# Kernel tuning notes

Measured on AMD Instinct MI355X. Metric: run time of the kernel, lower is better.

The kernel has to match this reference:

```python
import jax, jax.numpy as jnp
import numpy as np

N_QUBITS = 10
N_LAYERS = 4
BATCH = 512
FREQS = (1.0, 2.0, 4.0, 8.0, 16.0)
PI = float(np.pi)

# Combined CZ @ CNOT on (control, target), basis order |ct>
_CZCNOT = jnp.array([[1, 0, 0, 0],
                     [0, 1, 0, 0],
                     [0, 0, 0, -1],
                     [0, 0, 1, 0]], dtype=jnp.complex64)


def _apply_1q(state, U, q):
    # state: [B, 2,...,2]; U: [B,2,2] batched single-qubit gate on wire q
    s = jnp.moveaxis(state, q + 1, -1)
    s = jnp.einsum('b...i,bji->b...j', s, U)
    return jnp.moveaxis(s, -1, q + 1)


def _rz(state, phi, q):
    # diagonal gate: just multiply phases on the target axis
    s = jnp.moveaxis(state, q + 1, -1)
    h = phi * 0.5
    ph = jnp.stack([jnp.exp(-1j * h), jnp.exp(1j * h)], axis=-1).astype(jnp.complex64)  # [B,2]
    ph = ph.reshape(ph.shape[0], *([1] * (s.ndim - 2)), 2)
    return jnp.moveaxis(s * ph, -1, q + 1)


def _rx(state, th, q):
    c = jnp.cos(th * 0.5).astype(jnp.complex64)
    s_ = (-1j * jnp.sin(th * 0.5)).astype(jnp.complex64)
    U = jnp.stack([jnp.stack([c, s_], -1), jnp.stack([s_, c], -1)], -2)  # [B,2,2]
    return _apply_1q(state, U, q)


def _ry(state, th, q):
    c = jnp.cos(th * 0.5).astype(jnp.complex64)
    s_ = jnp.sin(th * 0.5).astype(jnp.complex64)
    U = jnp.stack([jnp.stack([c, -s_], -1), jnp.stack([s_, c], -1)], -2)
    return _apply_1q(state, U, q)


def _apply_2q(state, U4, c, t):
    # constant 4x4 gate on wires (c, t)
    s = jnp.moveaxis(state, (c + 1, t + 1), (-2, -1))
    shp = s.shape
    s = s.reshape(shp[:-2] + (4,))
    s = jnp.einsum('...i,ji->...j', s, U4)
    s = s.reshape(shp)
    return jnp.moveaxis(s, (-2, -1), (c + 1, t + 1))


def _forward(inputs, theta):
    B = inputs.shape[0]
    x = jnp.tanh(inputs)  # [B, n_feat]
    n_feat = x.shape[1]
    # |0...0> batched statevector [B, 2,...,2]
    state = jnp.zeros((B,) + (2,) * N_QUBITS, jnp.complex64)
    state = state.at[(slice(None),) + (0,) * N_QUBITS].set(1.0)
    # Fourier feature map: RZ(f*x), RX(0.5*f*x) per wire per frequency
    for q in range(N_QUBITS):
        xi = x[:, q % n_feat]
        for f in FREQS:
            state = _rz(state, f * xi, q)
            state = _rx(state, f * xi * 0.5, q)
    ang = jnp.tanh(theta) * PI  # [L, n, 3]
    for layer in range(N_LAYERS):
        for q in range(N_QUBITS):
            a = ang[layer, q]
            # qml.Rot(a0,a1,a2) = RZ(a0) -> RY(a1) -> RZ(a2), then RX(0.5*a0)
            state = _rz(state, jnp.broadcast_to(a[0], (B,)), q)
            state = _ry(state, jnp.broadcast_to(a[1], (B,)), q)
            state = _rz(state, jnp.broadcast_to(a[2], (B,)), q)
            state = _rx(state, jnp.broadcast_to(a[0] * 0.5, (B,)), q)
        for q in range(0, N_QUBITS - 1, 2):
            state = _apply_2q(state, _CZCNOT, q, q + 1)
        for q in range(1, N_QUBITS - 1, 2):
            state = _apply_2q(state, _CZCNOT, q, q + 1)
    # <Z_q> from probabilities
    p = jnp.abs(state) ** 2  # [B, 2,...,2] real
    exps = []
    for q in range(N_QUBITS):
        axes = tuple(a for a in range(1, N_QUBITS + 1) if a != q + 1)
        m = p.sum(axis=axes)  # [B,2]
        exps.append(m[:, 0] - m[:, 1])
    return jnp.stack(exps, axis=1).astype(jnp.float32)  # [B, n_qubits]


def setup_inputs() -> dict:
    key = jax.random.key(0)
    k1, k2 = jax.random.split(key)
    inputs = jax.random.normal(k1, (BATCH, N_QUBITS), dtype=jnp.float32)
    theta = jax.random.normal(k2, (N_LAYERS, N_QUBITS, 3), dtype=jnp.float32) * 0.1
    return {"inputs": inputs, "theta": theta}


def reference(inputs, theta):
    return _forward(inputs, theta)
```

## Files before the change

kernel.cpp:

```cpp
#include <hip/hip_runtime.h>
#include <math.h>

#define PI_F 3.14159265358979323846f

__device__ __forceinline__ float2 cmul(float2 a, float2 b) {
    return make_float2(a.x * b.x - a.y * b.y, a.x * b.y + a.y * b.x);
}
__device__ __forceinline__ float2 cfma(float2 u, float2 v, float2 acc) {
    acc.x = fmaf(u.x, v.x, fmaf(-u.y, v.y, acc.x));
    acc.y = fmaf(u.x, v.y, fmaf(u.y, v.x, acc.y));
    return acc;
}

__device__ __forceinline__ void gate_b0(float2 a[4], const float2* U) {
    float2 u00 = U[0], u01 = U[1], u10 = U[2], u11 = U[3];
    float2 n0 = cfma(u00, a[0], cmul(u01, a[1]));
    float2 n1 = cfma(u10, a[0], cmul(u11, a[1]));
    float2 n2 = cfma(u00, a[2], cmul(u01, a[3]));
    float2 n3 = cfma(u10, a[2], cmul(u11, a[3]));
    a[0] = n0; a[1] = n1; a[2] = n2; a[3] = n3;
}
__device__ __forceinline__ void gate_b1(float2 a[4], const float2* U) {
    float2 u00 = U[0], u01 = U[1], u10 = U[2], u11 = U[3];
    float2 n0 = cfma(u00, a[0], cmul(u01, a[2]));
    float2 n2 = cfma(u10, a[0], cmul(u11, a[2]));
    float2 n1 = cfma(u00, a[1], cmul(u01, a[3]));
    float2 n3 = cfma(u10, a[1], cmul(u11, a[3]));
    a[0] = n0; a[1] = n1; a[2] = n2; a[3] = n3;
}
__device__ __forceinline__ void gate_lane(float2 a[4], const float2* U, int p, int l) {
    int mask = 1 << p;
    bool h = (l >> p) & 1;
    float2 al = h ? U[3] : U[0];
    float2 be = h ? U[2] : U[1];
    #pragma unroll
    for (int r = 0; r < 4; r++) {
        float2 pa;
        pa.x = __shfl_xor(a[r].x, mask, 64);
        pa.y = __shfl_xor(a[r].y, mask, 64);
        a[r] = cfma(al, a[r], cmul(be, pa));
    }
}

__global__ __launch_bounds__(256) void qsim_fused(const float* __restrict__ inputs,
                                                  const float* __restrict__ theta,
                                                  float* __restrict__ out) {
    const int b = blockIdx.x;
    const int T = threadIdx.x;
    const int l = T & 63;
    const int w = T >> 6;

    __shared__ float2 sm[40][4];
    __shared__ float2 ve[10][2];
    __shared__ float2 vq[10][2];
    __shared__ float2 m4s[4][16];
    __shared__ __align__(16) float2 xch[2][1024];
    __shared__ float red[4][10];

    if (T < 40) {
        float a0 = tanhf(theta[T * 3 + 0]) * PI_F;
        float a1 = tanhf(theta[T * 3 + 1]) * PI_F;
        float a2 = tanhf(theta[T * 3 + 2]) * PI_F;
        float sz0, cz0; sincosf(a0 * 0.5f, &sz0, &cz0);
        float2 m00 = make_float2(cz0, -sz0);
        float2 m11 = make_float2(cz0,  sz0);
        float sy, cy; sincosf(a1 * 0.5f, &sy, &cy);
        float2 t00 = make_float2(cy * m00.x, cy * m00.y);
        float2 t01 = make_float2(-sy * m11.x, -sy * m11.y);
        float2 t10 = make_float2(sy * m00.x, sy * m00.y);
        float2 t11 = make_float2(cy * m11.x, cy * m11.y);
        float sz2, cz2; sincosf(a2 * 0.5f, &sz2, &cz2);
        float2 e0 = make_float2(cz2, -sz2), e1 = make_float2(cz2, sz2);
        t00 = cmul(e0, t00); t01 = cmul(e0, t01);
        t10 = cmul(e1, t10); t11 = cmul(e1, t11);
        float sx, cx; sincosf(a0 * 0.25f, &sx, &cx);
        sm[T][0] = make_float2(cx * t00.x + sx * t10.y, cx * t00.y - sx * t10.x);
        sm[T][1] = make_float2(cx * t01.x + sx * t11.y, cx * t01.y - sx * t11.x);
        sm[T][2] = make_float2(cx * t10.x + sx * t00.y, cx * t10.y - sx * t00.x);
        sm[T][3] = make_float2(cx * t11.x + sx * t01.y, cx * t11.y - sx * t01.x);
    } else if (T >= 64 && T < 74) {
        int q = T - 64;
        float x = tanhf(inputs[b * 10 + q]);
        float2 v0 = make_float2(1.f, 0.f), v1 = make_float2(0.f, 0.f);
        #pragma unroll
        for (int k = 0; k < 5; k++) {
            float phi = (float)(1 << k) * x;
            float sh, ch; sincosf(phi * 0.5f, &sh, &ch);
            float2 n0 = cmul(make_float2(ch, -sh), v0);
            float2 n1 = cmul(make_float2(ch,  sh), v1);
            float sx, cxx; sincosf(phi * 0.25f, &sx, &cxx);
            v0 = make_float2(cxx * n0.x + sx * n1.y, cxx * n0.y - sx * n1.x);
            v1 = make_float2(cxx * n1.x + sx * n0.y, cxx * n1.y - sx * n0.x);
        }
        ve[q][0] = v0; ve[q][1] = v1;
    }
    __syncthreads();
    if (T < 48) {
        int li = T >> 4, lyr = li + 1;
        int e = T & 15, row = e >> 2, col = e & 3;
        int sr = (row == 2) ? 3 : (row == 3) ? 2 : row;
        float sgn = (row == 2) ? -1.f : 1.f;
        float2 u0 = sm[lyr * 10 + 0][(sr >> 1) * 2 + (col >> 1)];
        float2 u1 = sm[lyr * 10 + 1][(sr & 1) * 2 + (col & 1)];
        float2 p = cmul(u0, u1);
        m4s[lyr][e] = make_float2(sgn * p.x, sgn * p.y);
    } else if (T >= 64 && T < 74) {
        int q = T - 64;
        float2 v0 = ve[q][0], v1 = ve[q][1];
        vq[q][0] = cfma(sm[q][0], v0, cmul(sm[q][1], v1));
        vq[q][1] = cfma(sm[q][2], v0, cmul(sm[q][3], v1));
    }
    __syncthreads();

    const int i0 = (w << 8) | (l << 2);
    float2 a[4];
    {
        int ii = i0;
        int f1 = (ii & 0x154) >> 1; int m = ii ^ f1;
        int f2 = (m & 0x2AA) >> 1;  int sh = m ^ f2;
        float2 P = vq[7][(sh >> 2) & 1];
        P = cmul(P, vq[6][(sh >> 3) & 1]);
        P = cmul(P, vq[5][(sh >> 4) & 1]);
        P = cmul(P, vq[4][(sh >> 5) & 1]);
        P = cmul(P, vq[3][(sh >> 6) & 1]);
        P = cmul(P, vq[2][(sh >> 7) & 1]);
        P = cmul(P, vq[1][(sh >> 8) & 1]);
        P = cmul(P, vq[0][(sh >> 9) & 1]);
        #pragma unroll
        for (int r = 0; r < 4; r++) {
            int i = i0 | r;
            int g1 = (i & 0x154) >> 1; int mm = i ^ g1;
            int g2 = (mm & 0x2AA) >> 1; int s = mm ^ g2;
            int neg = (__popc(g1 & ~i) + __popc(g2 & ~mm)) & 1;
            float2 t = cmul(vq[8][(s >> 1) & 1], vq[9][s & 1]);
            t = cmul(P, t);
            a[r] = neg ? make_float2(-t.x, -t.y) : t;
        }
    }

    int srcLane;
    float sg0, sg1, sg2, sg3;
    {
        #define CZP(r, SG) { int i = i0 | r; int g1 = (i & 0x154) >> 1; int mm = i ^ g1; \
                             int g2 = (mm & 0xAA) >> 1; int s = mm ^ g2; \
                             int neg = (__popc(g1 & ~i) + __popc(g2 & ~mm)) & 1; \
                             SG = neg ? -1.f : 1.f; if (r == 0) srcLane = (s >> 2) & 63; }
        CZP(0, sg0) CZP(1, sg1) CZP(2, sg2) CZP(3, sg3)
        #undef CZP
    }
    const bool L0 = l & 1;

    #pragma unroll
    for (int L = 1; L < 4; L++) {
        const float2 (*G)[4] = (const float2(*)[4])&sm[L * 10 + 2];
        gate_lane(a, G[0], 5, l);
        gate_lane(a, G[1], 4, l);
        gate_lane(a, G[2], 3, l);
        gate_lane(a, G[3], 2, l);
        gate_lane(a, G[4], 1, l);
        gate_lane(a, G[5], 0, l);
        gate_b1(a, G[6]);
        gate_b0(a, G[7]);
        {
            int buf = L & 1;
            float4* wp = (float4*)&xch[buf][T << 2];
            wp[0] = make_float4(a[0].x, a[0].y, a[1].x, a[1].y);
            wp[1] = make_float4(a[2].x, a[2].y, a[3].x, a[3].y);
            __syncthreads();
            const float2* M4row = &m4s[L][w * 4];
            float2 mw = M4row[w];
            float2 n[4];
            #pragma unroll
            for (int r = 0; r < 4; r++) n[r] = cmul(mw, a[r]);
            #pragma unroll
            for (int j = 0; j < 3; j++) {
                int wo = (w + 1 + j) & 3;
                float2 c = M4row[wo];
                const float4* rp = (const float4*)&xch[buf][(wo << 8) | (l << 2)];
                float4 v0 = rp[0], v1 = rp[1];
                n[0] = cfma(c, make_float2(v0.x, v0.y), n[0]);
                n[1] = cfma(c, make_float2(v0.z, v0.w), n[1]);
                n[2] = cfma(c, make_float2(v1.x, v1.y), n[2]);
                n[3] = cfma(c, make_float2(v1.z, v1.w), n[3]);
            }
            a[0] = n[0]; a[1] = n[1]; a[2] = n[2]; a[3] = n[3];
        }
        {
            float p0x = __shfl(a[0].x, srcLane, 64), p0y = __shfl(a[0].y, srcLane, 64);
            float p1x = __shfl(a[1].x, srcLane, 64), p1y = __shfl(a[1].y, srcLane, 64);
            float p2x = __shfl(a[2].x, srcLane, 64), p2y = __shfl(a[2].y, srcLane, 64);
            float p3x = __shfl(a[3].x, srcLane, 64), p3y = __shfl(a[3].y, srcLane, 64);
            a[0] = make_float2(sg0 * (L0 ? p3x : p0x), sg0 * (L0 ? p3y : p0y));
            a[1] = make_float2(sg1 * (L0 ? p2x : p1x), sg1 * (L0 ? p2y : p1y));
            a[2] = make_float2(sg2 * (L0 ? p0x : p3x), sg2 * (L0 ? p0y : p3y));
            a[3] = make_float2(sg3 * (L0 ? p1x : p2x), sg3 * (L0 ? p1y : p2y));
        }
    }

    float p0 = a[0].x * a[0].x + a[0].y * a[0].y;
    float p1 = a[1].x * a[1].x + a[1].y * a[1].y;
    float p2 = a[2].x * a[2].x + a[2].y * a[2].y;
    float p3 = a[3].x * a[3].x + a[3].y * a[3].y;
    float S = p0 + p1 + p2 + p3;
    float e[10];
    e[9] = p0 - p1 + p2 - p3;
    e[8] = p0 + p1 - p2 - p3;
    #pragma unroll
    for (int q = 2; q <= 7; q++) e[q] = ((l >> (7 - q)) & 1) ? -S : S;
    e[1] = (w & 1) ? -S : S;
    e[0] = (w & 2) ? -S : S;
    #pragma unroll
    for (int q = 0; q < 10; q++) {
        float v = e[q];
        #pragma unroll
        for (int off = 32; off > 0; off >>= 1) v += __shfl_down(v, off, 64);
        e[q] = v;
    }
    if ((T & 63) == 0) {
        #pragma unroll
        for (int q = 0; q < 10; q++) red[w][q] = e[q];
    }
    __syncthreads();
    if (T < 10) {
        out[b * 10 + T] = red[0][T] + red[1][T] + red[2][T] + red[3][T];
    }
}

extern "C" void kernel_launch(void* const* d_in, const int* in_sizes, int n_in,
                              void* d_out, int out_size, void* d_ws, size_t ws_size,
                              hipStream_t stream) {
    const float* inputs = (const float*)d_in[0];
    const float* theta  = (const float*)d_in[1];
    float* out = (float*)d_out;
    qsim_fused<<<512, 256, 0, stream>>>(inputs, theta, out);
}
```

Before: 16.19 us.

## Use DPP and permlane cross-lane ops, butterfly reduction, drop final CZ signs

Replaces ds_bpermute-based shuffles for lane bits 0, 1 and 5 with DPP quad permutes and permlane32_swap. The final expectation reduction becomes a single xor-butterfly that builds all per-bit differences at once, replacing ten separate 6-step shuffle reductions. Other changes: the feature-map sincos calls are replaced by double-angle recurrences, the phase product is computed as a tree, and the sign multiply is skipped in the last layer since signs do not affect probabilities. The aim is to cut LDS-crossbar shuffle traffic and reduction instructions, at the cost of small precision drift from the angle recurrence.

```diff
diff --git a/kernel.cpp b/kernel.cpp
--- a/kernel.cpp
+++ b/kernel.cpp
@@ -2,6 +2,8 @@
 #include <math.h>
 
 #define PI_F 3.14159265358979323846f
+
+typedef unsigned u32v2 __attribute__((ext_vector_type(2)));
 
 __device__ __forceinline__ float2 cmul(float2 a, float2 b) {
     return make_float2(a.x * b.x - a.y * b.y, a.x * b.y + a.y * b.x);
@@ -12,6 +14,62 @@
     return acc;
 }
 
+__device__ __forceinline__ float dpp_x1(float x) {
+    return __int_as_float(__builtin_amdgcn_update_dpp(0, __float_as_int(x), 0xB1, 0xF, 0xF, true));
+}
+__device__ __forceinline__ float dpp_x2(float x) {
+    return __int_as_float(__builtin_amdgcn_update_dpp(0, __float_as_int(x), 0x4E, 0xF, 0xF, true));
+}
+#if __has_builtin(__builtin_amdgcn_permlane32_swap)
+__device__ __forceinline__ float pl32(float x, int l) {
+    unsigned u = __float_as_uint(x);
+    u32v2 r = __builtin_amdgcn_permlane32_swap(u, u, false, false);
+    return __uint_as_float((l & 32) ? r.x : r.y);
+}
+#else
+__device__ __forceinline__ float pl32(float x, int l) { return __shfl_xor(x, 32, 64); }
+#endif
+
+__device__ __forceinline__ void gate_apply(float2 a[4], const float2 pa[4], float2 al, float2 be) {
+    #pragma unroll
+    for (int r = 0; r < 4; r++) a[r] = cfma(al, a[r], cmul(be, pa[r]));
+}
+__device__ __forceinline__ void gate_dpp1(float2 a[4], const float2* U, int l) {
+    bool h = l & 1;
+    float2 al = h ? U[3] : U[0], be = h ? U[2] : U[1];
+    float2 pa[4];
+    #pragma unroll
+    for (int r = 0; r < 4; r++) { pa[r].x = dpp_x1(a[r].x); pa[r].y = dpp_x1(a[r].y); }
+    gate_apply(a, pa, al, be);
+}
+__device__ __forceinline__ void gate_dpp2(float2 a[4], const float2* U, int l) {
+    bool h = l & 2;
+    float2 al = h ? U[3] : U[0], be = h ? U[2] : U[1];
+    float2 pa[4];
+    #pragma unroll
+    for (int r = 0; r < 4; r++) { pa[r].x = dpp_x2(a[r].x); pa[r].y = dpp_x2(a[r].y); }
+    gate_apply(a, pa, al, be);
+}
+__device__ __forceinline__ void gate_pl32(float2 a[4], const float2* U, int l) {
+    bool h = l & 32;
+    float2 al = h ? U[3] : U[0], be = h ? U[2] : U[1];
+    float2 pa[4];
+    #pragma unroll
+    for (int r = 0; r < 4; r++) { pa[r].x = pl32(a[r].x, l); pa[r].y = pl32(a[r].y, l); }
+    gate_apply(a, pa, al, be);
+}
+__device__ __forceinline__ void gate_shfl(float2 a[4], const float2* U, int p, int l) {
+    int mask = 1 << p;
+    bool h = (l >> p) & 1;
+    float2 al = h ? U[3] : U[0], be = h ? U[2] : U[1];
+    float2 pa[4];
+    #pragma unroll
+    for (int r = 0; r < 4; r++) {
+        pa[r].x = __shfl_xor(a[r].x, mask, 64);
+        pa[r].y = __shfl_xor(a[r].y, mask, 64);
+    }
+    gate_apply(a, pa, al, be);
+}
 __device__ __forceinline__ void gate_b0(float2 a[4], const float2* U) {
     float2 u00 = U[0], u01 = U[1], u10 = U[2], u11 = U[3];
     float2 n0 = cfma(u00, a[0], cmul(u01, a[1]));
@@ -27,19 +85,6 @@
     float2 n1 = cfma(u00, a[1], cmul(u01, a[3]));
     float2 n3 = cfma(u10, a[1], cmul(u11, a[3]));
     a[0] = n0; a[1] = n1; a[2] = n2; a[3] = n3;
-}
-__device__ __forceinline__ void gate_lane(float2 a[4], const float2* U, int p, int l) {
-    int mask = 1 << p;
-    bool h = (l >> p) & 1;
-    float2 al = h ? U[3] : U[0];
-    float2 be = h ? U[2] : U[1];
-    #pragma unroll
-    for (int r = 0; r < 4; r++) {
-        float2 pa;
-        pa.x = __shfl_xor(a[r].x, mask, 64);
-        pa.y = __shfl_xor(a[r].y, mask, 64);
-        a[r] = cfma(al, a[r], cmul(be, pa));
-    }
 }
 
 __global__ __launch_bounds__(256) void qsim_fused(const float* __restrict__ inputs,
@@ -81,16 +126,22 @@
     } else if (T >= 64 && T < 74) {
         int q = T - 64;
         float x = tanhf(inputs[b * 10 + q]);
+        float sA[6], cA[6];
+        sincosf(0.25f * x, &sA[0], &cA[0]);
+        #pragma unroll
+        for (int j = 1; j < 6; j++) {
+            sA[j] = 2.f * sA[j - 1] * cA[j - 1];
+            cA[j] = 1.f - 2.f * sA[j - 1] * sA[j - 1];
+        }
         float2 v0 = make_float2(1.f, 0.f), v1 = make_float2(0.f, 0.f);
         #pragma unroll
         for (int k = 0; k < 5; k++) {
-            float phi = (float)(1 << k) * x;
-            float sh, ch; sincosf(phi * 0.5f, &sh, &ch);
+            float sh = sA[k + 1], ch = cA[k + 1];
             float2 n0 = cmul(make_float2(ch, -sh), v0);
             float2 n1 = cmul(make_float2(ch,  sh), v1);
-            float sx, cxx; sincosf(phi * 0.25f, &sx, &cxx);
-            v0 = make_float2(cxx * n0.x + sx * n1.y, cxx * n0.y - sx * n1.x);
-            v1 = make_float2(cxx * n1.x + sx * n0.y, cxx * n1.y - sx * n0.x);
+            float sx = sA[k], cx = cA[k];
+            v0 = make_float2(cx * n0.x + sx * n1.y, cx * n0.y - sx * n1.x);
+            v1 = make_float2(cx * n1.x + sx * n0.y, cx * n1.y - sx * n0.x);
         }
         ve[q][0] = v0; ve[q][1] = v1;
     }
@@ -115,17 +166,13 @@
     const int i0 = (w << 8) | (l << 2);
     float2 a[4];
     {
-        int ii = i0;
-        int f1 = (ii & 0x154) >> 1; int m = ii ^ f1;
+        int f1 = (i0 & 0x154) >> 1; int m = i0 ^ f1;
         int f2 = (m & 0x2AA) >> 1;  int sh = m ^ f2;
-        float2 P = vq[7][(sh >> 2) & 1];
-        P = cmul(P, vq[6][(sh >> 3) & 1]);
-        P = cmul(P, vq[5][(sh >> 4) & 1]);
-        P = cmul(P, vq[4][(sh >> 5) & 1]);
-        P = cmul(P, vq[3][(sh >> 6) & 1]);
-        P = cmul(P, vq[2][(sh >> 7) & 1]);
-        P = cmul(P, vq[1][(sh >> 8) & 1]);
-        P = cmul(P, vq[0][(sh >> 9) & 1]);
+        float2 t76 = cmul(vq[7][(sh >> 2) & 1], vq[6][(sh >> 3) & 1]);
+        float2 t54 = cmul(vq[5][(sh >> 4) & 1], vq[4][(sh >> 5) & 1]);
+        float2 t32 = cmul(vq[3][(sh >> 6) & 1], vq[2][(sh >> 7) & 1]);
+        float2 t10 = cmul(vq[1][(sh >> 8) & 1], vq[0][(sh >> 9) & 1]);
+        float2 P = cmul(cmul(t76, t54), cmul(t32, t10));
         #pragma unroll
         for (int r = 0; r < 4; r++) {
             int i = i0 | r;
@@ -148,17 +195,17 @@
         CZP(0, sg0) CZP(1, sg1) CZP(2, sg2) CZP(3, sg3)
         #undef CZP
     }
-    const bool L0 = l & 1;
+    const bool Lb = l & 1;
 
     #pragma unroll
     for (int L = 1; L < 4; L++) {
         const float2 (*G)[4] = (const float2(*)[4])&sm[L * 10 + 2];
-        gate_lane(a, G[0], 5, l);
-        gate_lane(a, G[1], 4, l);
-        gate_lane(a, G[2], 3, l);
-        gate_lane(a, G[3], 2, l);
-        gate_lane(a, G[4], 1, l);
-        gate_lane(a, G[5], 0, l);
+        gate_pl32(a, G[0], l);
+        gate_shfl(a, G[1], 4, l);
+        gate_shfl(a, G[2], 3, l);
+        gate_shfl(a, G[3], 2, l);
+        gate_dpp2(a, G[4], l);
+        gate_dpp1(a, G[5], l);
         gate_b1(a, G[6]);
         gate_b0(a, G[7]);
         {
@@ -190,10 +237,17 @@
             float p1x = __shfl(a[1].x, srcLane, 64), p1y = __shfl(a[1].y, srcLane, 64);
             float p2x = __shfl(a[2].x, srcLane, 64), p2y = __shfl(a[2].y, srcLane, 64);
             float p3x = __shfl(a[3].x, srcLane, 64), p3y = __shfl(a[3].y, srcLane, 64);
-            a[0] = make_float2(sg0 * (L0 ? p3x : p0x), sg0 * (L0 ? p3y : p0y));
-            a[1] = make_float2(sg1 * (L0 ? p2x : p1x), sg1 * (L0 ? p2y : p1y));
-            a[2] = make_float2(sg2 * (L0 ? p0x : p3x), sg2 * (L0 ? p0y : p3y));
-            a[3] = make_float2(sg3 * (L0 ? p1x : p2x), sg3 * (L0 ? p1y : p2y));
+            if (L < 3) {
+                a[0] = make_float2(sg0 * (Lb ? p3x : p0x), sg0 * (Lb ? p3y : p0y));
+                a[1] = make_float2(sg1 * (Lb ? p2x : p1x), sg1 * (Lb ? p2y : p1y));
+                a[2] = make_float2(sg2 * (Lb ? p0x : p3x), sg2 * (Lb ? p0y : p3y));
+                a[3] = make_float2(sg3 * (Lb ? p1x : p2x), sg3 * (Lb ? p1y : p2y));
+            } else {
+                a[0] = make_float2(Lb ? p3x : p0x, Lb ? p3y : p0y);
+                a[1] = make_float2(Lb ? p2x : p1x, Lb ? p2y : p1y);
+                a[2] = make_float2(Lb ? p0x : p3x, Lb ? p0y : p3y);
+                a[3] = make_float2(Lb ? p1x : p2x, Lb ? p1y : p2y);
+            }
         }
     }
 
@@ -201,24 +255,40 @@
     float p1 = a[1].x * a[1].x + a[1].y * a[1].y;
     float p2 = a[2].x * a[2].x + a[2].y * a[2].y;
     float p3 = a[3].x * a[3].x + a[3].y * a[3].y;
-    float S = p0 + p1 + p2 + p3;
-    float e[10];
-    e[9] = p0 - p1 + p2 - p3;
-    e[8] = p0 + p1 - p2 - p3;
-    #pragma unroll
-    for (int q = 2; q <= 7; q++) e[q] = ((l >> (7 - q)) & 1) ? -S : S;
-    e[1] = (w & 1) ? -S : S;
-    e[0] = (w & 2) ? -S : S;
-    #pragma unroll
-    for (int q = 0; q < 10; q++) {
-        float v = e[q];
-        #pragma unroll
-        for (int off = 32; off > 0; off >>= 1) v += __shfl_down(v, off, 64);
-        e[q] = v;
-    }
-    if ((T & 63) == 0) {
-        #pragma unroll
-        for (int q = 0; q < 10; q++) red[w][q] = e[q];
+    float acc = p0 + p1 + p2 + p3;
+    float a8 = p0 + p1 - p2 - p3;
+    float a9 = p0 - p1 + p2 - p3;
+    float d0, d1, d2, d3, d4, d5;
+    { float pS = dpp_x1(acc); d0 = (l & 1) ? pS - acc : acc - pS; acc += pS;
+      a8 += dpp_x1(a8); a9 += dpp_x1(a9); }
+    { float pS = dpp_x2(acc); d1 = (l & 2) ? pS - acc : acc - pS; acc += pS;
+      a8 += dpp_x2(a8); a9 += dpp_x2(a9); d0 += dpp_x2(d0); }
+    { float pS = __shfl_xor(acc, 4, 64); d2 = (l & 4) ? pS - acc : acc - pS; acc += pS;
+      a8 += __shfl_xor(a8, 4, 64); a9 += __shfl_xor(a9, 4, 64);
+      d0 += __shfl_xor(d0, 4, 64); d1 += __shfl_xor(d1, 4, 64); }
+    { float pS = __shfl_xor(acc, 8, 64); d3 = (l & 8) ? pS - acc : acc - pS; acc += pS;
+      a8 += __shfl_xor(a8, 8, 64); a9 += __shfl_xor(a9, 8, 64);
+      d0 += __shfl_xor(d0, 8, 64); d1 += __shfl_xor(d1, 8, 64); d2 += __shfl_xor(d2, 8, 64); }
+    { float pS = __shfl_xor(acc, 16, 64); d4 = (l & 16) ? pS - acc : acc - pS; acc += pS;
+      a8 += __shfl_xor(a8, 16, 64); a9 += __shfl_xor(a9, 16, 64);
+      d0 += __shfl_xor(d0, 16, 64); d1 += __shfl_xor(d1, 16, 64);
+      d2 += __shfl_xor(d2, 16, 64); d3 += __shfl_xor(d3, 16, 64); }
+    { float pS = pl32(acc, l); d5 = (l & 32) ? pS - acc : acc - pS; acc += pS;
+      a8 += pl32(a8, l); a9 += pl32(a9, l);
+      d0 += pl32(d0, l); d1 += pl32(d1, l); d2 += pl32(d2, l);
+      d3 += pl32(d3, l); d4 += pl32(d4, l); }
+
+    if (l == 0) {
+        red[w][0] = (w & 2) ? -acc : acc;
+        red[w][1] = (w & 1) ? -acc : acc;
+        red[w][2] = d5;
+        red[w][3] = d4;
+        red[w][4] = d3;
+        red[w][5] = d2;
+        red[w][6] = d1;
+        red[w][7] = d0;
+        red[w][8] = a8;
+        red[w][9] = a9;
     }
     __syncthreads();
     if (T < 10) {
```

After: 16.42 us, median of 2. About the same (+1.4%).
